# Performance work log

Measured on AMD Instinct MI355X. Metric: run time of the kernel, lower is better.

## Reference

```python
import jax, jax.numpy as jnp
import numpy as np
import math

HIDDEN = 2048
N_HEADS = 16
HEAD_DIM = HIDDEN // N_HEADS  # 128
ROPE_THETA = 10000.0


def _rope_cos_sin(seq_len, dim, theta, dtype):
    # Megatron RotaryEmbedding: freqs = pos \outer inv_freq; emb = cat(freqs, freqs)
    inv_freq = 1.0 / (theta ** (jnp.arange(0, dim, 2, dtype=jnp.float32) / dim))
    pos = jnp.arange(seq_len, dtype=jnp.float32)
    freqs = jnp.outer(pos, inv_freq)            # [S, dim/2]
    emb = jnp.concatenate([freqs, freqs], -1)   # [S, dim]
    return jnp.cos(emb).astype(dtype), jnp.sin(emb).astype(dtype)


def _rotate_half(x):
    half = x.shape[-1] // 2
    return jnp.concatenate([-x[..., half:], x[..., :half]], axis=-1)


def setup_inputs() -> dict:
    key = jax.random.key(0)
    k1, k2, k3 = jax.random.split(key, 3)
    B, S = 2, 2048
    hidden_states = jax.random.normal(k1, (B, S, HIDDEN), dtype=jnp.float32)
    # torch Linear weights are [out_features, in_features]
    w_qkv = jax.random.normal(k2, (3 * HIDDEN, HIDDEN), dtype=jnp.float32) * (1.0 / math.sqrt(HIDDEN))
    w_o = jax.random.normal(k3, (HIDDEN, HIDDEN), dtype=jnp.float32) * (1.0 / math.sqrt(HIDDEN))
    return {"hidden_states": hidden_states, "w_qkv": w_qkv, "w_o": w_o}


def reference(hidden_states, w_qkv, w_o):
    B, S, H = hidden_states.shape
    # fused QKV projection: [B,S,H] @ [H, 3H] -> view (.., n_heads, 3, head_dim)
    mixed = jnp.einsum('bsh,oh->bso', hidden_states, w_qkv)
    mixed = mixed.reshape(B, S, N_HEADS, 3, HEAD_DIM)
    q, k, v = mixed[..., 0, :], mixed[..., 1, :], mixed[..., 2, :]  # [B,S,Hn,D]

    # fused split + RoPE (full rotary dim = head_dim)
    cos, sin = _rope_cos_sin(S, HEAD_DIM, ROPE_THETA, hidden_states.dtype)
    cos = cos[None, :, None, :]  # [1,S,1,D]
    sin = sin[None, :, None, :]
    q = q * cos + _rotate_half(q) * sin
    k = k * cos + _rotate_half(k) * sin

    # causal scaled-dot-product attention (flash_attn_func equivalent math)
    scale = 1.0 / math.sqrt(HEAD_DIM)
    scores = jnp.einsum('bqhd,bkhd->bhqk', q, k) * scale  # [B,Hn,S,S]
    causal = jnp.tril(jnp.ones((S, S), dtype=bool))
    scores = jnp.where(causal[None, None], scores, jnp.finfo(scores.dtype).min)
    probs = jax.nn.softmax(scores, axis=-1)
    attn = jnp.einsum('bhqk,bkhd->bqhd', probs, v)  # [B,S,Hn,D]

    attn = attn.reshape(B, S, H)
    out = jnp.einsum('bsh,oh->bso', attn, w_o)
    return out
```

## Files before the change

kernel.cpp:

```cpp
#include <hip/hip_runtime.h>
#include <hip/hip_bf16.h>
#include <cstdint>
#include <cstddef>

#define S_DIM 2048
#define H_DIM 2048
#define NHEAD 16
#define HD_DIM 128
#define O3    6144
#define BS    4096
#define NBH   32

typedef short  s16x8  __attribute__((ext_vector_type(8)));
typedef __bf16 bf16x8 __attribute__((ext_vector_type(8)));
typedef float  f32x4  __attribute__((ext_vector_type(4)));

__device__ __forceinline__ unsigned short f2bf(float f) {
  unsigned int b = __float_as_uint(f);
  b += 0x7FFFu + ((b >> 16) & 1u);
  return (unsigned short)(b >> 16);
}
__device__ __forceinline__ float bf2f(unsigned short u) {
  return __uint_as_float(((unsigned int)u) << 16);
}
__device__ __forceinline__ bf16x8 load8(const unsigned short* p) {
  s16x8 r = *(const s16x8*)p;
  return __builtin_bit_cast(bf16x8, r);
}
__device__ __forceinline__ f32x4 mfma_bf16(bf16x8 a, bf16x8 b, f32x4 c) {
  return __builtin_amdgcn_mfma_f32_16x16x32_bf16(a, b, c, 0, 0, 0);
}
__device__ __forceinline__ void gload_lds16(const void* g, void* l) {
  __builtin_amdgcn_global_load_lds(
      (__attribute__((address_space(1))) unsigned int*)g,
      (__attribute__((address_space(3))) unsigned int*)l, 16, 0, 0);
}

__global__ void cvt_kernel(const float* __restrict__ src,
                           unsigned short* __restrict__ dst, int n4) {
  int i = blockIdx.x * blockDim.x + threadIdx.x;
  int stride = gridDim.x * blockDim.x;
  for (; i < n4; i += stride) {
    float4 v = ((const float4*)src)[i];
    ushort4 o;
    o.x = f2bf(v.x); o.y = f2bf(v.y); o.z = f2bf(v.z); o.w = f2bf(v.w);
    ((ushort4*)dst)[i] = o;
  }
}

__global__ void rope_table_kernel(float* __restrict__ cosT,
                                  float* __restrict__ sinT) {
  int idx = blockIdx.x * blockDim.x + threadIdx.x;
  int s = idx >> 6, d = idx & 63;
  float inv = expf(-((float)d / 64.0f) * 9.210340371976184f);
  float ang = (float)s * inv;
  float sn, cs;
  sincosf(ang, &sn, &cs);
  cosT[idx] = cs;
  sinT[idx] = sn;
}

template <bool OUT_BF16, bool QKV_MAP>
__global__ __launch_bounds__(512, 1)
void gemm3b_kernel(const unsigned short* __restrict__ A,
                   const unsigned short* __restrict__ Bw,
                   void* __restrict__ C, int M, int N, int K) {
  __shared__ __align__(16) unsigned short lA[3][128 * 64];
  __shared__ __align__(16) unsigned short lB[3][256 * 64];
  const int tid  = threadIdx.x;
  const int wave = tid >> 6, lane = tid & 63;
  const int wm = wave >> 2, wn = wave & 3;
  const int lg = lane >> 4, ll = lane & 15;

  const int nbx = gridDim.x;
  const int id  = blockIdx.y * nbx + blockIdx.x;
  int m_tile, n_tile;
  if (QKV_MAP) {
    const int k = id & 7, q = id >> 3;
    const int ng = q >> 5, r = q & 31;
    m_tile = (k >> 1) * 8 + (r & 7);
    n_tile = (k & 1) * 12 + ng * 4 + (r >> 3);
  } else {
    const int nwg = gridDim.x * gridDim.y;
    const int swz = (id & 7) * (nwg >> 3) + (id >> 3);
    m_tile = swz / nbx;
    n_tile = swz % nbx;
  }
  const int m0 = m_tile * 128, n0 = n_tile * 256;

  f32x4 acc[4][4];
#pragma unroll
  for (int i = 0; i < 4; ++i)
#pragma unroll
    for (int j = 0; j < 4; ++j) acc[i][j] = (f32x4){0.f, 0.f, 0.f, 0.f};

  const unsigned short* aP[2];
  const unsigned short* bP[4];
  int aD[2], bD[4];
#pragma unroll
  for (int i = 0; i < 2; ++i) {
    int cb = (i * 8 + wave) * 64 + lane;
    int cs = cb ^ ((cb >> 3) & 7);
    aP[i] = A + (size_t)(m0 + (cs >> 3)) * K + (cs & 7) * 8;
    aD[i] = cb * 8;
  }
#pragma unroll
  for (int i = 0; i < 4; ++i) {
    int cb = (i * 8 + wave) * 64 + lane;
    int cs = cb ^ ((cb >> 3) & 7);
    bP[i] = Bw + (size_t)(n0 + (cs >> 3)) * K + (cs & 7) * 8;
    bD[i] = cb * 8;
  }

  auto STAGE = [&](int buf, int t) {
    const int kt = t << 6;
#pragma unroll
    for (int i = 0; i < 2; ++i) gload_lds16(aP[i] + kt, &lA[buf][aD[i]]);
#pragma unroll
    for (int i = 0; i < 4; ++i) gload_lds16(bP[i] + kt, &lB[buf][bD[i]]);
  };

  const int NT = K >> 6;
  STAGE(0, 0);
  if (NT > 1) {
    STAGE(1, 1);
    asm volatile("s_waitcnt vmcnt(6)" ::: "memory");
  } else {
    asm volatile("s_waitcnt vmcnt(0)" ::: "memory");
  }
  asm volatile("s_barrier" ::: "memory");

  for (int t = 0; t < NT; ++t) {
    const int cur = t % 3;
    const char* lAc = (const char*)&lA[cur][0];
    const char* lBc = (const char*)&lB[cur][0];

    bf16x8 af[4][2], bfr[2][2][2];
#pragma unroll
    for (int fq = 0; fq < 4; ++fq) {
      int r = wm * 64 + fq * 16 + ll;
#pragma unroll
      for (int kk = 0; kk < 2; ++kk) {
        int a = (r * 128 + kk * 64 + lg * 16) ^ ((r & 7) << 4);
        af[fq][kk] = load8((const unsigned short*)(lAc + a));
      }
    }
#pragma unroll
    for (int nh = 0; nh < 2; ++nh)
#pragma unroll
      for (int fq = 0; fq < 2; ++fq) {
        int r = wn * 64 + nh * 32 + fq * 16 + ll;
#pragma unroll
        for (int kk = 0; kk < 2; ++kk) {
          int a = (r * 128 + kk * 64 + lg * 16) ^ ((r & 7) << 4);
          bfr[nh][fq][kk] = load8((const unsigned short*)(lBc + a));
        }
      }

    if (t + 2 < NT) STAGE((t + 2) % 3, t + 2);

    __builtin_amdgcn_s_setprio(1);
#pragma unroll
    for (int nh = 0; nh < 2; ++nh)
#pragma unroll
      for (int fq = 0; fq < 4; ++fq)
#pragma unroll
        for (int gq = 0; gq < 2; ++gq)
#pragma unroll
          for (int kk = 0; kk < 2; ++kk)
            acc[fq][nh * 2 + gq] =
                mfma_bf16(af[fq][kk], bfr[nh][gq][kk], acc[fq][nh * 2 + gq]);
    __builtin_amdgcn_s_setprio(0);

    if (t + 2 < NT)
      asm volatile("s_waitcnt vmcnt(6)" ::: "memory");
    else if (t + 1 < NT)
      asm volatile("s_waitcnt vmcnt(0)" ::: "memory");
    asm volatile("s_barrier" ::: "memory");
  }

#pragma unroll
  for (int fm = 0; fm < 4; ++fm)
#pragma unroll
    for (int fn = 0; fn < 4; ++fn)
#pragma unroll
      for (int j = 0; j < 4; ++j) {
        int r   = m0 + wm * 64 + fm * 16 + lg * 4 + j;
        int col = n0 + wn * 64 + fn * 16 + ll;
        if (OUT_BF16)
          ((unsigned short*)C)[(size_t)r * N + col] = f2bf(acc[fm][fn][j]);
        else
          ((float*)C)[(size_t)r * N + col] = acc[fm][fn][j];
      }
}

__global__ void rope_qk_kernel(const unsigned short* __restrict__ mixed,
                               const float* __restrict__ cosT,
                               const float* __restrict__ sinT,
                               unsigned short* __restrict__ qr,
                               unsigned short* __restrict__ kr) {
  int m = blockIdx.x;
  int s = m & (S_DIM - 1);
  int b = m >> 11;
  const unsigned short* row = mixed + (size_t)m * O3;
#pragma unroll
  for (int it = 0; it < 4; ++it) {
    int idx = it * 256 + threadIdx.x;
    int h = idx >> 6, d = idx & 63;
    float c  = cosT[(s << 6) + d];
    float sn = sinT[(s << 6) + d];
    int base = h * 384;
    float q0 = bf2f(row[base + d]),       q1 = bf2f(row[base + 64 + d]);
    float k0 = bf2f(row[base + 128 + d]), k1 = bf2f(row[base + 192 + d]);
    size_t ob = ((size_t)(b * NHEAD + h) * S_DIM + s) * HD_DIM;
    qr[ob + d]      = f2bf(q0 * c - q1 * sn);
    qr[ob + 64 + d] = f2bf(q1 * c + q0 * sn);
    kr[ob + d]      = f2bf(k0 * c - k1 * sn);
    kr[ob + 64 + d] = f2bf(k1 * c + k0 * sn);
  }
}

__global__ __launch_bounds__(256)
void vtrans_kernel(const unsigned short* __restrict__ mixed,
                   unsigned short* __restrict__ vt) {
  __shared__ unsigned short t[64 * 65];
  int st = blockIdx.x, dt = blockIdx.y, bh = blockIdx.z;
  int b = bh >> 4, h = bh & 15;
  int s0 = st * 64, d0 = dt * 64;
  int tid = threadIdx.x;
#pragma unroll
  for (int it = 0; it < 2; ++it) {
    int c = it * 256 + tid;
    int sl = c >> 3, dc = c & 7;
    const unsigned short* src =
        mixed + (size_t)(b * S_DIM + s0 + sl) * O3 + h * 384 + 256 + d0 + dc * 8;
    s16x8 v = *(const s16x8*)src;
#pragma unroll
    for (int i = 0; i < 8; ++i) t[(dc * 8 + i) * 65 + sl] = (unsigned short)v[i];
  }
  __syncthreads();
#pragma unroll
  for (int it = 0; it < 2; ++it) {
    int c = it * 256 + tid;
    int dl = c >> 3, sc = c & 7;
    s16x8 v;
#pragma unroll
    for (int i = 0; i < 8; ++i) v[i] = (short)t[dl * 65 + sc * 8 + i];
    *(s16x8*)(vt + ((size_t)bh * HD_DIM + d0 + dl) * S_DIM + s0 + sc * 8) = v;
  }
}

__global__ __launch_bounds__(256, 2)
void attn_kernel(const unsigned short* __restrict__ qr,
                 const unsigned short* __restrict__ kr,
                 const unsigned short* __restrict__ vt,
                 unsigned short* __restrict__ out) {
  __shared__ __align__(16) unsigned short kbuf[2][64 * 128];
  __shared__ __align__(16) unsigned short vbuf[2][128 * 64];
  __shared__ __align__(16) unsigned short plds[4][16 * 72];
  const int p = blockIdx.x, bh = blockIdx.y;
  const int wave = threadIdx.x >> 6, lane = threadIdx.x & 63;
  const int b = bh >> 4, h = bh & 15;
  const int lg = lane >> 4, ll = lane & 15;
  const unsigned short* Qb = qr + (size_t)bh * S_DIM * HD_DIM;
  const unsigned short* Kb = kr + (size_t)bh * S_DIM * HD_DIM;
  const unsigned short* Vb = vt + (size_t)bh * HD_DIM * S_DIM;
  const float kE  = 0.12752792f;
  const float THR = 11.5416f;
  unsigned short* pw = &plds[wave][0];

  for (int seg = 0; seg < 2; ++seg) {
    const int qt = seg ? (31 - p) : p;
    const int qbase = qt * 64 + wave * 16;
    const int ntb = qt + 1;

    auto STAGE = [&](int buf, int t) {
      const int k0 = t * 64;
#pragma unroll
      for (int i = 0; i < 4; ++i) {
        int cb = (i * 4 + wave) * 64;
        int c  = cb + lane;
        int cs = c ^ ((c >> 4) & 7);
        gload_lds16(Kb + (size_t)(k0 + (cs >> 4)) * HD_DIM + (cs & 15) * 8,
                    &kbuf[buf][cb * 8]);
      }
#pragma unroll
      for (int i = 0; i < 4; ++i) {
        int cb = (i * 4 + wave) * 64;
        int c  = cb + lane;
        int cv = c ^ ((c >> 3) & 7);
        gload_lds16(Vb + (size_t)(cv >> 3) * S_DIM + k0 + (cv & 7) * 8,
                    &vbuf[buf][cb * 8]);
      }
    };

    bf16x8 aq[4];
#pragma unroll
    for (int kk = 0; kk < 4; ++kk)
      aq[kk] = load8(Qb + (size_t)(qbase + ll) * HD_DIM + kk * 32 + lg * 8);

    float mk[4], lsum[4];
    f32x4 o[8];
#pragma unroll
    for (int j = 0; j < 4; ++j) { mk[j] = -1e30f; lsum[j] = 0.f; }
#pragma unroll
    for (int f = 0; f < 8; ++f) o[f] = (f32x4){0.f, 0.f, 0.f, 0.f};

    STAGE(0, 0);
    __syncthreads();

    for (int t = 0; t < ntb; ++t) {
      const int cur = t & 1;
      if (t + 1 < ntb) STAGE(cur ^ 1, t + 1);
      const int k0 = t * 64;
      const bool diag = (t == ntb - 1);

      f32x4 s[4];
#pragma unroll
      for (int kf = 0; kf < 4; ++kf) s[kf] = (f32x4){0.f, 0.f, 0.f, 0.f};
      const char* kb = (const char*)&kbuf[cur][0];
      __builtin_amdgcn_s_setprio(1);
#pragma unroll
      for (int kf = 0; kf < 4; ++kf) {
        int r = kf * 16 + ll;
#pragma unroll
        for (int kk = 0; kk < 4; ++kk) {
          int a = (r * 256 + kk * 64 + lg * 16) ^ ((r & 7) << 4);
          s[kf] = mfma_bf16(aq[kk], load8((const unsigned short*)(kb + a)), s[kf]);
        }
      }
      __builtin_amdgcn_s_setprio(0);

      if (diag) {
#pragma unroll
        for (int kf = 0; kf < 4; ++kf) {
          int kcol = k0 + kf * 16 + ll;
#pragma unroll
          for (int j = 0; j < 4; ++j) {
            int qrow = qbase + lg * 4 + j;
            if (kcol > qrow) s[kf][j] = -1e31f;
          }
        }
      }

      float pmax[4];
      bool ok = true;
#pragma unroll
      for (int j = 0; j < 4; ++j) {
        pmax[j] = fmaxf(fmaxf(s[0][j], s[1][j]), fmaxf(s[2][j], s[3][j]));
        ok = ok && (pmax[j] * kE - mk[j] <= THR);
      }
      if (!__all(ok)) {
#pragma unroll
        for (int j = 0; j < 4; ++j) {
          float rm = pmax[j] * kE;
#pragma unroll
          for (int off = 1; off < 16; off <<= 1)
            rm = fmaxf(rm, __shfl_xor(rm, off, 64));
          rm = fmaxf(rm, mk[j]);
          float corr = exp2f(mk[j] - rm);
          mk[j] = rm;
          lsum[j] *= corr;
#pragma unroll
          for (int f = 0; f < 8; ++f) o[f][j] *= corr;
        }
      }
#pragma unroll
      for (int j = 0; j < 4; ++j) {
        int prow = (lg * 4 + j) * 72;
#pragma unroll
        for (int kf = 0; kf < 4; ++kf) {
          float e = exp2f(fmaf(s[kf][j], kE, -mk[j]));
          lsum[j] += e;
          pw[prow + kf * 16 + ll] = f2bf(e);
        }
      }

      bf16x8 pa0 = load8(&pw[ll * 72 + lg * 8]);
      bf16x8 pa1 = load8(&pw[ll * 72 + 32 + lg * 8]);
      const char* vb = (const char*)&vbuf[cur][0];
      __builtin_amdgcn_s_setprio(1);
#pragma unroll
      for (int f = 0; f < 8; ++f) {
        int rv = f * 16 + ll;
        int a0 = (rv * 128 + lg * 16) ^ ((rv & 7) << 4);
        int a1 = (rv * 128 + 64 + lg * 16) ^ ((rv & 7) << 4);
        o[f] = mfma_bf16(pa0, load8((const unsigned short*)(vb + a0)), o[f]);
        o[f] = mfma_bf16(pa1, load8((const unsigned short*)(vb + a1)), o[f]);
      }
      __builtin_amdgcn_s_setprio(0);

      __syncthreads();
    }

#pragma unroll
    for (int j = 0; j < 4; ++j) {
      float l = lsum[j];
#pragma unroll
      for (int off = 1; off < 16; off <<= 1) l += __shfl_xor(l, off, 64);
      lsum[j] = 1.0f / l;
    }
#pragma unroll
    for (int f = 0; f < 8; ++f)
#pragma unroll
      for (int j = 0; j < 4; ++j) {
        int srow = qbase + lg * 4 + j;
        out[((size_t)(b * S_DIM + srow)) * H_DIM + h * HD_DIM + f * 16 + ll] =
            f2bf(o[f][j] * lsum[j]);
      }
  }
}

extern "C" void kernel_launch(void* const* d_in, const int* in_sizes, int n_in,
                              void* d_out, int out_size, void* d_ws, size_t ws_size,
                              hipStream_t stream) {
  (void)in_sizes; (void)n_in; (void)out_size; (void)ws_size;
  const float* hidden = (const float*)d_in[0];
  const float* wqkv   = (const float*)d_in[1];
  const float* wo     = (const float*)d_in[2];
  char* ws = (char*)d_ws;
  unsigned short* hid_b  = (unsigned short*)(ws);
  unsigned short* wqkv_b = (unsigned short*)(ws + 16777216);
  unsigned short* wo_b   = (unsigned short*)(ws + 41943040);
  unsigned short* mixed  = (unsigned short*)(ws + 50331648);
  unsigned short* q_r    = (unsigned short*)(ws + 100663296);
  unsigned short* k_r    = (unsigned short*)(ws + 117440512);
  unsigned short* v_t    = (unsigned short*)(ws + 134217728);
  unsigned short* attn   = (unsigned short*)(ws + 150994944);
  float* cosT            = (float*)(ws + 167772160);
  float* sinT            = (float*)(ws + 168296448);

  cvt_kernel<<<1024, 256, 0, stream>>>(hidden, hid_b, BS * H_DIM / 4);
  cvt_kernel<<<1024, 256, 0, stream>>>(wqkv, wqkv_b, O3 * H_DIM / 4);
  cvt_kernel<<<1024, 256, 0, stream>>>(wo, wo_b, H_DIM * H_DIM / 4);
  rope_table_kernel<<<S_DIM * 64 / 256, 256, 0, stream>>>(cosT, sinT);

  gemm3b_kernel<true, true><<<dim3(O3 / 256, BS / 128), 512, 0, stream>>>(
      hid_b, wqkv_b, mixed, BS, O3, H_DIM);

  rope_qk_kernel<<<BS, 256, 0, stream>>>(mixed, cosT, sinT, q_r, k_r);
  vtrans_kernel<<<dim3(32, 2, 32), 256, 0, stream>>>(mixed, v_t);

  attn_kernel<<<dim3(16, 32), 256, 0, stream>>>(q_r, k_r, v_t, attn);

  gemm3b_kernel<false, false><<<dim3(H_DIM / 256, BS / 128), 512, 0, stream>>>(
      attn, wo_b, d_out, BS, H_DIM, H_DIM);
}
```

Before: 274.5 us.

## Load GEMM A operand directly into registers and double-buffer B in LDS

The GEMM kernel no longer stages the A tile through shared memory. Each wave loads its A fragments straight from global memory into registers, alternating between even and odd register sets, while B goes through a two-buffer LDS pipeline instead of three. This drops LDS traffic and frees shared memory for A. In exchange it uses more registers, loses the LDS swizzle sharing of A between the four waves in each wave row (each A element is now fetched from global/L2 four times), and waits on vmcnt(0) every step, which shortens the prefetch distance.

```diff
diff --git a/kernel.cpp b/kernel.cpp
--- a/kernel.cpp
+++ b/kernel.cpp
@@ -62,11 +62,10 @@
 
 template <bool OUT_BF16, bool QKV_MAP>
 __global__ __launch_bounds__(512, 1)
-void gemm3b_kernel(const unsigned short* __restrict__ A,
-                   const unsigned short* __restrict__ Bw,
-                   void* __restrict__ C, int M, int N, int K) {
-  __shared__ __align__(16) unsigned short lA[3][128 * 64];
-  __shared__ __align__(16) unsigned short lB[3][256 * 64];
+void gemm_areg_kernel(const unsigned short* __restrict__ A,
+                      const unsigned short* __restrict__ Bw,
+                      void* __restrict__ C, int M, int N, int K) {
+  __shared__ __align__(16) unsigned short lB[2][256 * 64];
   const int tid  = threadIdx.x;
   const int wave = tid >> 6, lane = tid & 63;
   const int wm = wave >> 2, wn = wave & 3;
@@ -94,16 +93,24 @@
 #pragma unroll
     for (int j = 0; j < 4; ++j) acc[i][j] = (f32x4){0.f, 0.f, 0.f, 0.f};
 
-  const unsigned short* aP[2];
+  const unsigned short* Ab = A + (size_t)m0 * K;
+  int aRow[4], aCol[2];
+#pragma unroll
+  for (int fq = 0; fq < 4; ++fq) aRow[fq] = (wm * 64 + fq * 16 + ll) * K;
+#pragma unroll
+  for (int kk = 0; kk < 2; ++kk) aCol[kk] = kk * 32 + lg * 8;
+
+  bf16x8 afE[4][2], afO[4][2];
+  auto LDA = [&](bf16x8 (&d)[4][2], int kt) {
+#pragma unroll
+    for (int fq = 0; fq < 4; ++fq)
+#pragma unroll
+      for (int kk = 0; kk < 2; ++kk)
+        d[fq][kk] = load8(Ab + aRow[fq] + kt + aCol[kk]);
+  };
+
   const unsigned short* bP[4];
-  int aD[2], bD[4];
-#pragma unroll
-  for (int i = 0; i < 2; ++i) {
-    int cb = (i * 8 + wave) * 64 + lane;
-    int cs = cb ^ ((cb >> 3) & 7);
-    aP[i] = A + (size_t)(m0 + (cs >> 3)) * K + (cs & 7) * 8;
-    aD[i] = cb * 8;
-  }
+  int bD[4];
 #pragma unroll
   for (int i = 0; i < 4; ++i) {
     int cb = (i * 8 + wave) * 64 + lane;
@@ -111,40 +118,14 @@
     bP[i] = Bw + (size_t)(n0 + (cs >> 3)) * K + (cs & 7) * 8;
     bD[i] = cb * 8;
   }
-
-  auto STAGE = [&](int buf, int t) {
-    const int kt = t << 6;
-#pragma unroll
-    for (int i = 0; i < 2; ++i) gload_lds16(aP[i] + kt, &lA[buf][aD[i]]);
+  auto STB = [&](int buf, int kt) {
 #pragma unroll
     for (int i = 0; i < 4; ++i) gload_lds16(bP[i] + kt, &lB[buf][bD[i]]);
   };
 
-  const int NT = K >> 6;
-  STAGE(0, 0);
-  if (NT > 1) {
-    STAGE(1, 1);
-    asm volatile("s_waitcnt vmcnt(6)" ::: "memory");
-  } else {
-    asm volatile("s_waitcnt vmcnt(0)" ::: "memory");
-  }
-  asm volatile("s_barrier" ::: "memory");
-
-  for (int t = 0; t < NT; ++t) {
-    const int cur = t % 3;
-    const char* lAc = (const char*)&lA[cur][0];
-    const char* lBc = (const char*)&lB[cur][0];
-
-    bf16x8 af[4][2], bfr[2][2][2];
-#pragma unroll
-    for (int fq = 0; fq < 4; ++fq) {
-      int r = wm * 64 + fq * 16 + ll;
-#pragma unroll
-      for (int kk = 0; kk < 2; ++kk) {
-        int a = (r * 128 + kk * 64 + lg * 16) ^ ((r & 7) << 4);
-        af[fq][kk] = load8((const unsigned short*)(lAc + a));
-      }
-    }
+  auto BODY = [&](int buf, bf16x8 (&af)[4][2]) {
+    const char* lBc = (const char*)&lB[buf][0];
+    bf16x8 bfr[2][2][2];
 #pragma unroll
     for (int nh = 0; nh < 2; ++nh)
 #pragma unroll
@@ -156,9 +137,6 @@
           bfr[nh][fq][kk] = load8((const unsigned short*)(lBc + a));
         }
       }
-
-    if (t + 2 < NT) STAGE((t + 2) % 3, t + 2);
-
     __builtin_amdgcn_s_setprio(1);
 #pragma unroll
     for (int nh = 0; nh < 2; ++nh)
@@ -171,11 +149,26 @@
             acc[fq][nh * 2 + gq] =
                 mfma_bf16(af[fq][kk], bfr[nh][gq][kk], acc[fq][nh * 2 + gq]);
     __builtin_amdgcn_s_setprio(0);
-
-    if (t + 2 < NT)
-      asm volatile("s_waitcnt vmcnt(6)" ::: "memory");
-    else if (t + 1 < NT)
-      asm volatile("s_waitcnt vmcnt(0)" ::: "memory");
+  };
+
+  const int NT = K >> 6;
+  STB(0, 0);
+  LDA(afE, 0);
+  asm volatile("s_waitcnt vmcnt(0)" ::: "memory");
+  asm volatile("s_barrier" ::: "memory");
+
+  for (int t = 0; t < NT; t += 2) {
+    LDA(afO, (t + 1) << 6);
+    STB(1, (t + 1) << 6);
+    BODY(0, afE);
+    asm volatile("s_waitcnt vmcnt(0)" ::: "memory");
+    asm volatile("s_barrier" ::: "memory");
+    if (t + 2 < NT) {
+      LDA(afE, (t + 2) << 6);
+      STB(0, (t + 2) << 6);
+    }
+    BODY(1, afO);
+    asm volatile("s_waitcnt vmcnt(0)" ::: "memory");
     asm volatile("s_barrier" ::: "memory");
   }
 
@@ -435,7 +428,7 @@
   cvt_kernel<<<1024, 256, 0, stream>>>(wo, wo_b, H_DIM * H_DIM / 4);
   rope_table_kernel<<<S_DIM * 64 / 256, 256, 0, stream>>>(cosT, sinT);
 
-  gemm3b_kernel<true, true><<<dim3(O3 / 256, BS / 128), 512, 0, stream>>>(
+  gemm_areg_kernel<true, true><<<dim3(O3 / 256, BS / 128), 512, 0, stream>>>(
       hid_b, wqkv_b, mixed, BS, O3, H_DIM);
 
   rope_qk_kernel<<<BS, 256, 0, stream>>>(mixed, cosT, sinT, q_r, k_r);
@@ -443,6 +436,6 @@
 
   attn_kernel<<<dim3(16, 32), 256, 0, stream>>>(q_r, k_r, v_t, attn);
 
-  gemm3b_kernel<false, false><<<dim3(H_DIM / 256, BS / 128), 512, 0, stream>>>(
+  gemm_areg_kernel<false, false><<<dim3(H_DIM / 256, BS / 128), 512, 0, stream>>>(
       attn, wo_b, d_out, BS, H_DIM, H_DIM);
 }
```

Measured after the change: 461.2 us. +68.0%, slower.
